# Performance work log

Hardware: AMD Instinct MI355X
Metric: run time of the kernel (lower is better)

Reference implementation:

```python
import jax, jax.numpy as jnp
import numpy as np

QLEN, BSZ, D_MODEL = 1024, 4, 1024
N_HEAD, D_HEAD = 16, 64
NEG = -1e30


def _layer_norm(x, g, b, eps=1e-5):
    mu = jnp.mean(x, axis=-1, keepdims=True)
    var = jnp.mean((x - mu) ** 2, axis=-1, keepdims=True)
    return (x - mu) / jnp.sqrt(var + eps) * g + b


def _rel_shift(x):
    # x: [qlen, klen, bsz, n_head] -- Transformer-XL relative shift
    q, k, b, n = x.shape
    x = jnp.pad(x, ((0, 0), (1, 0), (0, 0), (0, 0)))  # zero-pad along klen front
    x = x.reshape(k + 1, q, b, n)[1:]
    return x.reshape(q, k, b, n)


def setup_inputs() -> dict:
    key = jax.random.key(0)
    ks = jax.random.split(key, 8)
    s = 0.02
    w = jax.random.normal(ks[0], (QLEN, BSZ, D_MODEL), jnp.float32)
    r = jax.random.normal(ks[1], (QLEN, D_MODEL), jnp.float32)
    r_w_bias = jax.random.normal(ks[2], (N_HEAD, D_HEAD), jnp.float32) * s
    r_r_bias = jax.random.normal(ks[3], (N_HEAD, D_HEAD), jnp.float32) * s
    attn_mask = jnp.tril(jnp.ones((QLEN, QLEN), dtype=bool))  # causal: True = attend
    W_qkv = jax.random.normal(ks[4], (D_MODEL, 3 * N_HEAD * D_HEAD), jnp.float32) * s
    W_r = jax.random.normal(ks[5], (D_MODEL, N_HEAD * D_HEAD), jnp.float32) * s
    W_o = jax.random.normal(ks[6], (N_HEAD * D_HEAD, D_MODEL), jnp.float32) * s
    gamma = jnp.ones((D_MODEL,), jnp.float32)
    beta = jnp.zeros((D_MODEL,), jnp.float32)
    return {"w": w, "r": r, "r_w_bias": r_w_bias, "r_r_bias": r_r_bias,
            "attn_mask": attn_mask, "W_qkv": W_qkv, "W_r": W_r, "W_o": W_o,
            "gamma": gamma, "beta": beta}


def reference(w, r, r_w_bias, r_r_bias, attn_mask, W_qkv, W_r, W_o, gamma, beta):
    qlen, bsz, _ = w.shape
    scale = 1.0 / (D_HEAD ** 0.5)
    heads = w @ W_qkv                                    # [q, b, 3*n*d]
    q_h, k_h, v_h = jnp.split(heads, 3, axis=-1)
    q_h = q_h.reshape(qlen, bsz, N_HEAD, D_HEAD)
    k_h = k_h.reshape(qlen, bsz, N_HEAD, D_HEAD)
    v_h = v_h.reshape(qlen, bsz, N_HEAD, D_HEAD)
    r_k = (r @ W_r).reshape(-1, N_HEAD, D_HEAD)          # [rlen, n, d]
    AC = jnp.einsum('ibnd,jbnd->ijbn', q_h + r_w_bias, k_h)
    BD = jnp.einsum('ibnd,jnd->ijbn', q_h + r_r_bias, r_k)
    BD = _rel_shift(BD)
    score = (AC + BD) * scale                            # [q, k, b, n]
    score = jnp.where(attn_mask[:, :, None, None], score, NEG)
    prob = jax.nn.softmax(score, axis=1)
    vec = jnp.einsum('ijbn,jbnd->ibnd', prob, v_h).reshape(qlen, bsz, N_HEAD * D_HEAD)
    attn_out = vec @ W_o
    return _layer_norm(w + attn_out, gamma, beta)
```

## Files before the change

kernel.cpp:

```cpp
#include <hip/hip_runtime.h>
#include <math.h>

constexpr int QLEN_C  = 1024;
constexpr int BSZ_C   = 4;
constexpr int DMODEL  = 1024;
constexpr float SCALE = 0.125f;
constexpr float NEGF  = -1e30f;

typedef __attribute__((ext_vector_type(8))) short bh8;
typedef __attribute__((ext_vector_type(4))) float f32x4;

__device__ inline short f2bf(float f) {
    union { float f; unsigned u; } v; v.f = f;
    unsigned r = v.u + 0x7FFFu + ((v.u >> 16) & 1u);
    return (short)(r >> 16);
}
__device__ inline float bf2f(short s) {
    union { unsigned u; float f; } v;
    v.u = ((unsigned)(unsigned short)s) << 16;
    return v.f;
}
__device__ inline void gload16(const void* g, void* l) {
    __builtin_amdgcn_global_load_lds(
        (__attribute__((address_space(1))) void*)g,
        (__attribute__((address_space(3))) void*)l, 16, 0, 0);
}
__device__ inline void wave_lds_fence() {
    __builtin_amdgcn_sched_barrier(0);
    __builtin_amdgcn_s_waitcnt(0xC07F);
    __builtin_amdgcn_sched_barrier(0);
}
__device__ inline void block_sync() {
    __builtin_amdgcn_sched_barrier(0);
    __builtin_amdgcn_s_barrier();
    __builtin_amdgcn_sched_barrier(0);
}
__device__ inline void wait_vm8() {
    __builtin_amdgcn_sched_barrier(0);
    asm volatile("s_waitcnt vmcnt(8)" ::: "memory");
    __builtin_amdgcn_sched_barrier(0);
}
__device__ inline void wait_vm6() {
    __builtin_amdgcn_sched_barrier(0);
    asm volatile("s_waitcnt vmcnt(6)" ::: "memory");
    __builtin_amdgcn_sched_barrier(0);
}
__device__ inline void wait_vm0() {
    __builtin_amdgcn_sched_barrier(0);
    asm volatile("s_waitcnt vmcnt(0)" ::: "memory");
    __builtin_amdgcn_sched_barrier(0);
}

__global__ __launch_bounds__(512, 2)
void gemm12_8ph(const short* __restrict__ wb, const short* __restrict__ WqkvT,
                short* __restrict__ headsb,
                const short* __restrict__ rb, const short* __restrict__ WrT,
                short* __restrict__ rkb)
{
    constexpr int NT = 16;
    __shared__ alignas(16) short Ald[2][2][128][64];
    __shared__ alignas(16) short Bld[2][2][128][64];

    const int bid0 = blockIdx.x;
    const int bid = (bid0 & 7) * 26 + (bid0 >> 3);

    const short* A; const short* BT; short* Cc; int Nn; int bx, by;
    if (bid < 192) {
        A = wb; BT = WqkvT; Cc = headsb; Nn = 3072;
        bx = bid % 12; by = bid / 12;
    } else {
        int q = bid - 192;
        A = rb; BT = WrT; Cc = rkb; Nn = 1024;
        bx = q & 3; by = q >> 2;
    }
    const int row0 = by * 256, col0 = bx * 256;

    const int tid = threadIdx.x;
    const int wid = tid >> 6, lane = tid & 63;
    const int quad = lane >> 4, c = lane & 15;
    const int wr = wid >> 2, wcn = wid & 3;
    const int hb = wcn >> 1;

    auto stage_half = [&](short* dst, const short* src, int srcRow0, int kcol) {
        const int r0 = tid >> 3, b0 = tid & 7;
        gload16(src + (size_t)(srcRow0 + r0) * 1024 + kcol + ((b0 ^ (r0 & 7)) * 8),
                (char*)dst + tid * 16);
        const int t2 = tid + 512;
        const int r1 = t2 >> 3, b1 = t2 & 7;
        gload16(src + (size_t)(srcRow0 + r1) * 1024 + kcol + ((b1 ^ (r1 & 7)) * 8),
                (char*)dst + t2 * 16);
    };

    f32x4 acc[8][4];
    #pragma unroll
    for (int mf = 0; mf < 8; ++mf)
        #pragma unroll
        for (int nf = 0; nf < 4; ++nf) acc[mf][nf] = (f32x4)0.0f;

    stage_half(&Ald[0][0][0][0], A, row0,        0);
    stage_half(&Ald[0][1][0][0], A, row0 + 128,  0);
    stage_half(&Bld[0][0][0][0], BT, col0,       0);
    stage_half(&Bld[0][1][0][0], BT, col0 + 128, 0);
    stage_half(&Ald[1][0][0][0], A, row0,        64);
    stage_half(&Ald[1][1][0][0], A, row0 + 128,  64);
    stage_half(&Bld[1][0][0][0], BT, col0,       64);
    stage_half(&Bld[1][1][0][0], BT, col0 + 128, 64);
    wait_vm8();
    block_sync();

    for (int t = 0; t < NT; ++t) {
        const int d = t & 1;

        bh8 aF[8][2], bF[4][2];
        #pragma unroll
        for (int mf = 0; mf < 8; ++mf)
            #pragma unroll
            for (int ks = 0; ks < 2; ++ks)
                aF[mf][ks] = *(const bh8*)&Ald[d][wr][mf * 16 + c]
                                 [((ks * 4 + quad) ^ (c & 7)) * 8];
        #pragma unroll
        for (int nf = 0; nf < 4; ++nf)
            #pragma unroll
            for (int ks = 0; ks < 2; ++ks)
                bF[nf][ks] = *(const bh8*)&Bld[d][hb][(wcn & 1) * 64 + nf * 16 + c]
                                 [((ks * 4 + quad) ^ (c & 7)) * 8];

        wave_lds_fence();
        block_sync();

        const int ts = t + 2;

        __builtin_amdgcn_s_setprio(1);
        #pragma unroll
        for (int mf = 0; mf < 4; ++mf)
            #pragma unroll
            for (int nf = 0; nf < 2; ++nf) {
                acc[mf][nf] = __builtin_amdgcn_mfma_f32_16x16x32_bf16(aF[mf][0], bF[nf][0], acc[mf][nf], 0, 0, 0);
                acc[mf][nf] = __builtin_amdgcn_mfma_f32_16x16x32_bf16(aF[mf][1], bF[nf][1], acc[mf][nf], 0, 0, 0);
            }
        __builtin_amdgcn_s_setprio(0);

        if (ts < NT) {
            stage_half(&Ald[d][0][0][0], A, row0,       ts * 64);
            stage_half(&Ald[d][1][0][0], A, row0 + 128, ts * 64);
        }

        __builtin_amdgcn_s_setprio(1);
        #pragma unroll
        for (int mf = 0; mf < 4; ++mf)
            #pragma unroll
            for (int nf = 2; nf < 4; ++nf) {
                acc[mf][nf] = __builtin_amdgcn_mfma_f32_16x16x32_bf16(aF[mf][0], bF[nf][0], acc[mf][nf], 0, 0, 0);
                acc[mf][nf] = __builtin_amdgcn_mfma_f32_16x16x32_bf16(aF[mf][1], bF[nf][1], acc[mf][nf], 0, 0, 0);
            }
        __builtin_amdgcn_s_setprio(0);

        if (ts < NT) {
            stage_half(&Bld[d][0][0][0], BT, col0,       ts * 64);
            stage_half(&Bld[d][1][0][0], BT, col0 + 128, ts * 64);
        }

        __builtin_amdgcn_s_setprio(1);
        #pragma unroll
        for (int mf = 4; mf < 8; ++mf)
            #pragma unroll
            for (int nf = 0; nf < 2; ++nf) {
                acc[mf][nf] = __builtin_amdgcn_mfma_f32_16x16x32_bf16(aF[mf][0], bF[nf][0], acc[mf][nf], 0, 0, 0);
                acc[mf][nf] = __builtin_amdgcn_mfma_f32_16x16x32_bf16(aF[mf][1], bF[nf][1], acc[mf][nf], 0, 0, 0);
            }
        #pragma unroll
        for (int mf = 4; mf < 8; ++mf)
            #pragma unroll
            for (int nf = 2; nf < 4; ++nf) {
                acc[mf][nf] = __builtin_amdgcn_mfma_f32_16x16x32_bf16(aF[mf][0], bF[nf][0], acc[mf][nf], 0, 0, 0);
                acc[mf][nf] = __builtin_amdgcn_mfma_f32_16x16x32_bf16(aF[mf][1], bF[nf][1], acc[mf][nf], 0, 0, 0);
            }
        __builtin_amdgcn_s_setprio(0);

        if (t + 2 < NT)      wait_vm8();
        else if (t + 1 < NT) wait_vm0();
        if (t + 1 < NT)      block_sync();
    }

    wave_lds_fence();
    block_sync();
    short* cst = &Ald[0][0][0][0];
    const int crow = tid >> 2, cseg = tid & 3;
    #pragma unroll
    for (int pass = 0; pass < 2; ++pass) {
        if (wr == pass) {
            #pragma unroll
            for (int mf = 0; mf < 8; ++mf)
                #pragma unroll
                for (int nf = 0; nf < 4; ++nf)
                    #pragma unroll
                    for (int rr = 0; rr < 4; ++rr)
                        cst[(mf * 16 + quad * 4 + rr) * 256 + wcn * 64 + nf * 16 + c] =
                            f2bf(acc[mf][nf][rr]);
        }
        wave_lds_fence();
        block_sync();
        {
            short* gp = Cc + (size_t)(row0 + pass * 128 + crow) * Nn + col0 + cseg * 64;
            const short* lp = &cst[crow * 256 + cseg * 64];
            #pragma unroll
            for (int u = 0; u < 8; ++u)
                *(bh8*)(gp + u * 8) = *(const bh8*)(lp + u * 8);
        }
        if (pass == 0) { wave_lds_fence(); block_sync(); }
    }
}

__global__ __launch_bounds__(512, 2)
void gemm_wo_8ph(const short* __restrict__ A, const short* __restrict__ BT,
                 float* __restrict__ C0, float* __restrict__ C1)
{
    constexpr int NT = 8;
    constexpr int N  = 1024;
    __shared__ alignas(16) short Ald[2][2][128][64];
    __shared__ alignas(16) short Bld[2][128][64];

    const int bid0 = blockIdx.x;
    const int bid = (bid0 & 7) * 32 + (bid0 >> 3);
    const int half = bid & 1, tile = bid >> 1;
    const int by = tile >> 3, bx = tile & 7;
    const int row0 = by * 256, col0 = bx * 128;
    const int k_lo = half * 512;
    float* C = half ? C1 : C0;

    const int tid = threadIdx.x;
    const int wid = tid >> 6, lane = tid & 63;
    const int quad = lane >> 4, c = lane & 15;
    const int wr = wid >> 2, wcn = wid & 3;

    auto stage_half = [&](short* dst, const short* src, int srcRow0, int kcol) {
        const int r0 = tid >> 3, b0 = tid & 7;
        gload16(src + (size_t)(srcRow0 + r0) * 1024 + kcol + ((b0 ^ (r0 & 7)) * 8),
                (char*)dst + tid * 16);
        const int t2 = tid + 512;
        const int r1 = t2 >> 3, b1 = t2 & 7;
        gload16(src + (size_t)(srcRow0 + r1) * 1024 + kcol + ((b1 ^ (r1 & 7)) * 8),
                (char*)dst + t2 * 16);
    };

    f32x4 acc[8][2];
    #pragma unroll
    for (int mf = 0; mf < 8; ++mf)
        #pragma unroll
        for (int nf = 0; nf < 2; ++nf) acc[mf][nf] = (f32x4)0.0f;

    stage_half(&Ald[0][0][0][0], A, row0,        k_lo);
    stage_half(&Ald[0][1][0][0], A, row0 + 128,  k_lo);
    stage_half(&Bld[0][0][0],    BT, col0,       k_lo);
    stage_half(&Ald[1][0][0][0], A, row0,        k_lo + 64);
    stage_half(&Ald[1][1][0][0], A, row0 + 128,  k_lo + 64);
    stage_half(&Bld[1][0][0],    BT, col0,       k_lo + 64);
    wait_vm6();
    block_sync();

    for (int t = 0; t < NT; ++t) {
        const int d = t & 1;

        bh8 aF[8][2], bF[2][2];
        #pragma unroll
        for (int mf = 0; mf < 8; ++mf)
            #pragma unroll
            for (int ks = 0; ks < 2; ++ks)
                aF[mf][ks] = *(const bh8*)&Ald[d][wr][mf * 16 + c]
                                 [((ks * 4 + quad) ^ (c & 7)) * 8];
        #pragma unroll
        for (int nf = 0; nf < 2; ++nf)
            #pragma unroll
            for (int ks = 0; ks < 2; ++ks)
                bF[nf][ks] = *(const bh8*)&Bld[d][wcn * 32 + nf * 16 + c]
                                 [((ks * 4 + quad) ^ (c & 7)) * 8];

        wave_lds_fence();
        block_sync();

        const int ts = t + 2;
        const int kc = k_lo + ts * 64;

        __builtin_amdgcn_s_setprio(1);
        #pragma unroll
        for (int mf = 0; mf < 4; ++mf)
            #pragma unroll
            for (int nf = 0; nf < 2; ++nf) {
                acc[mf][nf] = __builtin_amdgcn_mfma_f32_16x16x32_bf16(aF[mf][0], bF[nf][0], acc[mf][nf], 0, 0, 0);
                acc[mf][nf] = __builtin_amdgcn_mfma_f32_16x16x32_bf16(aF[mf][1], bF[nf][1], acc[mf][nf], 0, 0, 0);
            }
        __builtin_amdgcn_s_setprio(0);

        if (ts < NT) {
            stage_half(&Ald[d][0][0][0], A, row0,       kc);
            stage_half(&Ald[d][1][0][0], A, row0 + 128, kc);
        }

        __builtin_amdgcn_s_setprio(1);
        #pragma unroll
        for (int mf = 4; mf < 6; ++mf)
            #pragma unroll
            for (int nf = 0; nf < 2; ++nf) {
                acc[mf][nf] = __builtin_amdgcn_mfma_f32_16x16x32_bf16(aF[mf][0], bF[nf][0], acc[mf][nf], 0, 0, 0);
                acc[mf][nf] = __builtin_amdgcn_mfma_f32_16x16x32_bf16(aF[mf][1], bF[nf][1], acc[mf][nf], 0, 0, 0);
            }
        __builtin_amdgcn_s_setprio(0);

        if (ts < NT) stage_half(&Bld[d][0][0], BT, col0, kc);

        __builtin_amdgcn_s_setprio(1);
        #pragma unroll
        for (int mf = 6; mf < 8; ++mf)
            #pragma unroll
            for (int nf = 0; nf < 2; ++nf) {
                acc[mf][nf] = __builtin_amdgcn_mfma_f32_16x16x32_bf16(aF[mf][0], bF[nf][0], acc[mf][nf], 0, 0, 0);
                acc[mf][nf] = __builtin_amdgcn_mfma_f32_16x16x32_bf16(aF[mf][1], bF[nf][1], acc[mf][nf], 0, 0, 0);
            }
        __builtin_amdgcn_s_setprio(0);

        if (t + 2 < NT)      wait_vm6();
        else if (t + 1 < NT) wait_vm0();
        if (t + 1 < NT)      block_sync();
    }

    #pragma unroll
    for (int mf = 0; mf < 8; ++mf)
        #pragma unroll
        for (int nf = 0; nf < 2; ++nf)
            #pragma unroll
            for (int rr = 0; rr < 4; ++rr) {
                int orow = row0 + wr * 128 + mf * 16 + quad * 4 + rr;
                int ocol = col0 + wcn * 32 + nf * 16 + c;
                C[(size_t)orow * N + ocol] = acc[mf][nf][rr];
            }
}

__device__ inline void transp_tile(const float* __restrict__ B, short* __restrict__ BT,
                                   int K, int N, int n0, int k0, int t,
                                   float (*tile)[68])
{
    const int row = t >> 2, c4 = t & 3;
    const float* src = B + (size_t)(k0 + row) * N + n0 + c4 * 16;
    #pragma unroll
    for (int u = 0; u < 4; ++u) {
        float4 v = *(const float4*)(src + u * 4);
        tile[row][c4 * 16 + u * 4 + 0] = v.x;
        tile[row][c4 * 16 + u * 4 + 1] = v.y;
        tile[row][c4 * 16 + u * 4 + 2] = v.z;
        tile[row][c4 * 16 + u * 4 + 3] = v.w;
    }
    __syncthreads();
    const int nl = t >> 2, kc = t & 3;
    short tmp[16];
    #pragma unroll
    for (int e = 0; e < 16; ++e) tmp[e] = f2bf(tile[kc * 16 + e][nl]);
    short* dst = BT + (size_t)(n0 + nl) * K + k0 + kc * 16;
    *(bh8*)dst = *(bh8*)&tmp[0];
    *(bh8*)(dst + 8) = *(bh8*)&tmp[8];
}

__global__ __launch_bounds__(256)
void prep_all(const float* __restrict__ w, const float* __restrict__ r,
              const float* __restrict__ Wqkv, const float* __restrict__ Wr,
              const float* __restrict__ Wo,
              short* __restrict__ wb, short* __restrict__ rb,
              short* __restrict__ WqkvT, short* __restrict__ WrT,
              short* __restrict__ WoT, short* __restrict__ rkb)
{
    __shared__ float tile[64][68];
    const int bid = blockIdx.x;
    const int t = threadIdx.x;

    if (bid < 2048) {
        int idx = (bid * 256 + t) * 8;
        bh8 o;
        #pragma unroll
        for (int e = 0; e < 8; ++e) o[e] = f2bf(w[idx + e]);
        *(bh8*)(wb + idx) = o;
    } else if (bid < 2560) {
        int idx = ((bid - 2048) * 256 + t) * 8;
        bh8 o;
        #pragma unroll
        for (int e = 0; e < 8; ++e) o[e] = f2bf(r[idx + e]);
        *(bh8*)(rb + idx) = o;
    } else if (bid < 3328) {
        int tt = bid - 2560;
        transp_tile(Wqkv, WqkvT, 1024, 3072, (tt % 48) * 64, (tt / 48) * 64, t, tile);
    } else if (bid < 3584) {
        int tt = bid - 3328;
        transp_tile(Wr, WrT, 1024, 1024, (tt % 16) * 64, (tt / 16) * 64, t, tile);
    } else if (bid < 3840) {
        int tt = bid - 3584;
        transp_tile(Wo, WoT, 1024, 1024, (tt % 16) * 64, (tt / 16) * 64, t, tile);
    } else {
        int idx = 1024 * 1024 + ((bid - 3840) * 256 + t) * 8;
        bh8 z;
        #pragma unroll
        for (int e = 0; e < 8; ++e) z[e] = 0;
        *(bh8*)(rkb + idx) = z;
    }
}

__global__ __launch_bounds__(256)
void prep_kv2(const short* __restrict__ headsb, const short* __restrict__ rkb,
              short* __restrict__ kfrag, short* __restrict__ vfrag,
              short* __restrict__ rfrag)
{
    __shared__ short vtile[64][72];
    const int blk = blockIdx.x;
    const int t = threadIdx.x;

    if (blk < 1024) {
        const int bn = blk >> 4, ju = blk & 15;
        const int b = bn & 3, nn = bn >> 2;
        const int j0 = ju * 64;
        const int row = t >> 2, d0 = (t & 3) * 16;

        const short* kp = headsb + ((size_t)(j0 + row) * 4 + b) * 3072 + 1024 + nn * 64 + d0;
        const short* vp = kp + 1024;
        bh8 k0 = *(const bh8*)kp, k1 = *(const bh8*)(kp + 8);
        bh8 v0 = *(const bh8*)vp, v1 = *(const bh8*)(vp + 8);

        {
            const int jtile = (j0 + row) >> 4, cc = row & 15;
            short* kb_bn = kfrag + (size_t)bn * 65536 + (size_t)jtile * 1024 + cc * 8;
            const int d1 = d0 + 8;
            *(bh8*)(kb_bn + (d0 >> 5) * 512 + ((d0 >> 3) & 3) * 128) = k0;
            *(bh8*)(kb_bn + (d1 >> 5) * 512 + ((d1 >> 3) & 3) * 128) = k1;
        }
        #pragma unroll
        for (int e = 0; e < 8; ++e) {
            vtile[row][d0 + e] = v0[e];
            vtile[row][d0 + 8 + e] = v1[e];
        }
        __syncthreads();
        const int d = t >> 2, jl0 = (t & 3) * 16;
        short tmp[16];
        #pragma unroll
        for (int e = 0; e < 16; ++e) tmp[e] = vtile[jl0 + e][d];
        short* vb = vfrag + (size_t)bn * 65536 + (size_t)ju * 4096
                  + (d >> 4) * 1024 + (d & 15) * 8;
        const int jl1 = jl0 + 8;
        *(bh8*)(vb + (jl0 >> 5) * 512 + ((jl0 >> 3) & 3) * 128) = *(bh8*)&tmp[0];
        *(bh8*)(vb + (jl1 >> 5) * 512 + ((jl1 >> 3) & 3) * 128) = *(bh8*)&tmp[8];
    } else {
        const int rblk = blk - 1024;
        const int row = rblk * 4 + (t >> 6);
        const int col0 = (t & 63) * 16;
        const short* src = rkb + (size_t)row * 1024 + col0;
        bh8 r0 = *(const bh8*)src, r1 = *(const bh8*)(src + 8);
        const int rt = row >> 4, cc = row & 15;
        const int nn = col0 >> 6, dd = col0 & 63, dd1 = dd + 8;
        short* dst = rfrag + (size_t)rt * 16384 + nn * 1024 + cc * 8;
        *(bh8*)(dst + (dd  >> 5) * 512 + ((dd  >> 3) & 3) * 128) = r0;
        *(bh8*)(dst + (dd1 >> 5) * 512 + ((dd1 >> 3) & 3) * 128) = r1;
    }
}

__global__ __launch_bounds__(256)
void attn_mfma(const short* __restrict__ headsb, const short* __restrict__ rfrag,
               const short* __restrict__ kfrag, const short* __restrict__ vfrag,
               const float* __restrict__ rwb, const float* __restrict__ rrb,
               short* __restrict__ vecb)
{
    __shared__ alignas(16) short sP[4][2][16 * 80];

    const int tid = threadIdx.x;
    const int wave = tid >> 6, lane = tid & 63;
    const int quad = lane >> 4, c = lane & 15;

    const int bi = blockIdx.x;
    const int itile = 15 - (bi >> 6);
    const int bn = bi & 63;
    const int n = bn >> 2, b = bn & 3;
    const int nU = itile + 1;
    const int rb = itile * 64 + wave * 16;

    const int dq = n * 64 + quad * 8;
    const short* kbp = kfrag + (size_t)bn * 65536;
    const short* vtp = vfrag + (size_t)bn * 65536;
    const int lin = quad * 128 + c * 8;

    bh8 ones;
    #pragma unroll
    for (int e = 0; e < 8; ++e) ones[e] = (short)0x3F80;

    bh8 aAC[2], aBD[2];
    #pragma unroll
    for (int ks = 0; ks < 2; ++ks) {
        const short* qp = headsb + ((size_t)(rb + c) * 4 + b) * 3072 + dq + 32 * ks;
        bh8 q8 = *(const bh8*)qp;
        #pragma unroll
        for (int e = 0; e < 8; ++e) {
            float qv = bf2f(q8[e]);
            aAC[ks][e] = f2bf(qv + rwb[dq + 32 * ks + e]);
            aBD[ks][e] = f2bf(qv + rrb[dq + 32 * ks + e]);
        }
    }

    bh8 rkv[10], kbv[8];
    auto pf = [&](int j0) {
        const int rt0 = (1008 - rb + j0) >> 4;
        #pragma unroll
        for (int tt = 0; tt < 5; ++tt) {
            const short* rp = rfrag + (size_t)(rt0 + tt) * 16384 + n * 1024 + lin;
            rkv[2 * tt]     = *(const bh8*)rp;
            rkv[2 * tt + 1] = *(const bh8*)(rp + 512);
        }
        const int jt0 = j0 >> 4;
        #pragma unroll
        for (int jt = 0; jt < 4; ++jt) {
            const short* kp = kbp + (size_t)(jt0 + jt) * 1024 + lin;
            kbv[2 * jt]     = *(const bh8*)kp;
            kbv[2 * jt + 1] = *(const bh8*)(kp + 512);
        }
    };

    f32x4 oacc[4], lacc;
    #pragma unroll
    for (int dt = 0; dt < 4; ++dt) oacc[dt] = (f32x4)0.0f;
    lacc = (f32x4)0.0f;

    pf(0);
    int j0 = 0;

    for (int u = 0; u < nU; ++u) {
        short* PL = &sP[wave][u & 1][0];

        bh8 vvv[8];
        {
            const short* vup = vtp + (size_t)(j0 >> 6) * 4096;
            #pragma unroll
            for (int dt = 0; dt < 4; ++dt) {
                const short* vp = vup + dt * 1024 + lin;
                vvv[2 * dt]     = *(const bh8*)vp;
                vvv[2 * dt + 1] = *(const bh8*)(vp + 512);
            }
        }

        f32x4 bt[5];
        #pragma unroll
        for (int tt = 0; tt < 5; ++tt) {
            bt[tt] = (f32x4)0.0f;
            bt[tt] = __builtin_amdgcn_mfma_f32_16x16x32_bf16(aBD[0], rkv[2 * tt], bt[tt], 0, 0, 0);
            bt[tt] = __builtin_amdgcn_mfma_f32_16x16x32_bf16(aBD[1], rkv[2 * tt + 1], bt[tt], 0, 0, 0);
        }
        f32x4 ac[4];
        #pragma unroll
        for (int jt = 0; jt < 4; ++jt) {
            ac[jt] = (f32x4)0.0f;
            ac[jt] = __builtin_amdgcn_mfma_f32_16x16x32_bf16(aAC[0], kbv[2 * jt], ac[jt], 0, 0, 0);
            ac[jt] = __builtin_amdgcn_mfma_f32_16x16x32_bf16(aAC[1], kbv[2 * jt + 1], ac[jt], 0, 0, 0);
        }

        if (u + 1 < nU) pf(j0 + 64);

        #pragma unroll
        for (int r = 0; r < 4; ++r) {
            const int row = quad * 4 + r;
            const int o = 15 - row;
            const int src = (lane & 48) | ((c + o) & 15);
            const int gi = rb + row;
            #pragma unroll
            for (int jt = 0; jt < 4; ++jt) {
                float sval = (c < o) ? bt[jt + 1][r] : bt[jt][r];
                float bd = __shfl(sval, src, 64);
                int gj = j0 + c + 16 * jt;
                float v = SCALE * (ac[jt][r] + bd);
                PL[row * 80 + c + 16 * jt] = (gj > gi) ? (short)0 : f2bf(__expf(v));
            }
        }

        wave_lds_fence();

        bh8 aP[2];
        #pragma unroll
        for (int ks = 0; ks < 2; ++ks)
            aP[ks] = *(const bh8*)(PL + c * 80 + 32 * ks + quad * 8);
        #pragma unroll
        for (int dt = 0; dt < 4; ++dt) {
            oacc[dt] = __builtin_amdgcn_mfma_f32_16x16x32_bf16(aP[0], vvv[2 * dt], oacc[dt], 0, 0, 0);
            oacc[dt] = __builtin_amdgcn_mfma_f32_16x16x32_bf16(aP[1], vvv[2 * dt + 1], oacc[dt], 0, 0, 0);
        }
        lacc = __builtin_amdgcn_mfma_f32_16x16x32_bf16(aP[0], ones, lacc, 0, 0, 0);
        lacc = __builtin_amdgcn_mfma_f32_16x16x32_bf16(aP[1], ones, lacc, 0, 0, 0);

        j0 += 64;
    }

    #pragma unroll
    for (int r = 0; r < 4; ++r) {
        float rinv = 1.f / lacc[r];
        int gi = rb + quad * 4 + r;
        short* op = vecb + ((size_t)gi * 4 + b) * 1024 + n * 64;
        #pragma unroll
        for (int dt = 0; dt < 4; ++dt)
            op[c + 16 * dt] = f2bf(oacc[dt][r] * rinv);
    }
}

__global__ __launch_bounds__(256)
void ln_kernel(const float* __restrict__ w, const float* __restrict__ a0,
               const float* __restrict__ a1,
               const float* __restrict__ gamma, const float* __restrict__ beta,
               float* __restrict__ out)
{
    const int row = blockIdx.x;
    const int tid = threadIdx.x;
    const float4* xw4 = (const float4*)(w  + (size_t)row * DMODEL);
    const float4* p04 = (const float4*)(a0 + (size_t)row * DMODEL);
    const float4* p14 = (const float4*)(a1 + (size_t)row * DMODEL);

    float4 a = xw4[tid], b0 = p04[tid], b1 = p14[tid];
    float x[4] = {a.x + b0.x + b1.x, a.y + b0.y + b1.y,
                  a.z + b0.z + b1.z, a.w + b0.w + b1.w};
    float s = x[0] + x[1] + x[2] + x[3];

    __shared__ float red[6];
    #pragma unroll
    for (int m = 1; m < 64; m <<= 1) s += __shfl_xor(s, m, 64);
    int wv = tid >> 6, lnid = tid & 63;
    if (lnid == 0) red[wv] = s;
    __syncthreads();
    if (tid == 0) red[4] = red[0] + red[1] + red[2] + red[3];
    __syncthreads();
    float mu = red[4] * (1.f / DMODEL);

    float vs = 0.f;
    #pragma unroll
    for (int e = 0; e < 4; ++e) { float d = x[e] - mu; vs += d * d; }
    #pragma unroll
    for (int m = 1; m < 64; m <<= 1) vs += __shfl_xor(vs, m, 64);
    if (lnid == 0) red[wv] = vs;
    __syncthreads();
    if (tid == 0) red[5] = red[0] + red[1] + red[2] + red[3];
    __syncthreads();
    float var = red[5] * (1.f / DMODEL);
    float inv = rsqrtf(var + 1e-5f);

    float4 g = ((const float4*)gamma)[tid];
    float4 be = ((const float4*)beta)[tid];
    float4 o;
    o.x = (x[0] - mu) * inv * g.x + be.x;
    o.y = (x[1] - mu) * inv * g.y + be.y;
    o.z = (x[2] - mu) * inv * g.z + be.z;
    o.w = (x[3] - mu) * inv * g.w + be.w;
    ((float4*)(out + (size_t)row * DMODEL))[tid] = o;
}

extern "C" void kernel_launch(void* const* d_in, const int* in_sizes, int n_in,
                              void* d_out, int out_size, void* d_ws, size_t ws_size,
                              hipStream_t stream)
{
    const float* w     = (const float*)d_in[0];
    const float* r     = (const float*)d_in[1];
    const float* rwb   = (const float*)d_in[2];
    const float* rrb   = (const float*)d_in[3];
    const float* Wqkv  = (const float*)d_in[5];
    const float* Wr    = (const float*)d_in[6];
    const float* Wo    = (const float*)d_in[7];
    const float* gamma = (const float*)d_in[8];
    const float* beta  = (const float*)d_in[9];
    float* out = (float*)d_out;

    short* headsb = (short*)d_ws;
    short* wb     = headsb + 12582912;
    short* WqkvT  = wb + 4194304;
    short* rb     = WqkvT + 3145728;
    short* WrT    = rb + 1048576;
    short* WoT    = WrT + 1048576;
    short* rkb    = WoT + 1048576;
    short* kfrag  = rkb + 1114112;
    short* vfrag  = kfrag + 4194304;
    short* vecb   = vfrag + 4194304;

    short* rfrag  = rb;

    float* attno0 = (float*)headsb;
    float* attno1 = (float*)wb;

    prep_all<<<3872, 256, 0, stream>>>(w, r, Wqkv, Wr, Wo, wb, rb, WqkvT, WrT, WoT, rkb);
    gemm12_8ph<<<dim3(208), 512, 0, stream>>>(wb, WqkvT, headsb, rb, WrT, rkb);
    prep_kv2<<<dim3(1296), 256, 0, stream>>>(headsb, rkb, kfrag, vfrag, rfrag);
    attn_mfma<<<dim3(1024), 256, 0, stream>>>(headsb, rfrag, kfrag, vfrag, rwb, rrb, vecb);
    gemm_wo_8ph<<<dim3(256), 512, 0, stream>>>(vecb, WoT, attno0, attno1);
    ln_kernel<<<4096, 256, 0, stream>>>(w, attno0, attno1, gamma, beta, out);
}
```

Before: 127.6 us.

## Split long causal attention rows into two KV halves and combine partials

Query tiles 8-15 now have their key range split into two tasks, giving 24 tasks per head/batch instead of 16. The split tasks write unnormalized partial outputs and row sums to scratch, and a new combine kernel adds them and normalizes. The aim is to balance the triangular workload across the grid and shorten the tail of long-row blocks. It also moves the causal mask check onto the diagonal tile only, and rearranges the rfrag fragments in place instead of copying them. The cost is an extra launch plus fp32 partial traffic; the in-place shuffle relies on each block only touching its own tile.

```diff
diff --git a/kernel.cpp b/kernel.cpp
--- a/kernel.cpp
+++ b/kernel.cpp
@@ -5,7 +5,6 @@
 constexpr int BSZ_C   = 4;
 constexpr int DMODEL  = 1024;
 constexpr float SCALE = 0.125f;
-constexpr float NEGF  = -1e30f;
 
 typedef __attribute__((ext_vector_type(8))) short bh8;
 typedef __attribute__((ext_vector_type(4))) float f32x4;
@@ -402,9 +401,8 @@
 }
 
 __global__ __launch_bounds__(256)
-void prep_kv2(const short* __restrict__ headsb, const short* __restrict__ rkb,
-              short* __restrict__ kfrag, short* __restrict__ vfrag,
-              short* __restrict__ rfrag)
+void prep_kv2(const short* __restrict__ headsb, short* __restrict__ rfrag,
+              short* __restrict__ kfrag, short* __restrict__ vfrag)
 {
     __shared__ short vtile[64][72];
     const int blk = blockIdx.x;
@@ -444,24 +442,33 @@
         *(bh8*)(vb + (jl0 >> 5) * 512 + ((jl0 >> 3) & 3) * 128) = *(bh8*)&tmp[0];
         *(bh8*)(vb + (jl1 >> 5) * 512 + ((jl1 >> 3) & 3) * 128) = *(bh8*)&tmp[8];
     } else {
-        const int rblk = blk - 1024;
-        const int row = rblk * 4 + (t >> 6);
-        const int col0 = (t & 63) * 16;
-        const short* src = rkb + (size_t)row * 1024 + col0;
-        bh8 r0 = *(const bh8*)src, r1 = *(const bh8*)(src + 8);
-        const int rt = row >> 4, cc = row & 15;
-        const int nn = col0 >> 6, dd = col0 & 63, dd1 = dd + 8;
-        short* dst = rfrag + (size_t)rt * 16384 + nn * 1024 + cc * 8;
-        *(bh8*)(dst + (dd  >> 5) * 512 + ((dd  >> 3) & 3) * 128) = r0;
-        *(bh8*)(dst + (dd1 >> 5) * 512 + ((dd1 >> 3) & 3) * 128) = r1;
-    }
-}
+        const int rt = blk - 1024;
+        short* base = rfrag + (size_t)rt * 16384;
+        const int cc = t >> 4, nn = t & 15;
+        const short* src = base + cc * 1024 + nn * 64;
+        bh8 v[8];
+        #pragma unroll
+        for (int i = 0; i < 8; ++i) v[i] = *(const bh8*)(src + i * 8);
+        __syncthreads();
+        short* dst = base + nn * 1024 + cc * 8;
+        #pragma unroll
+        for (int ks = 0; ks < 2; ++ks)
+            #pragma unroll
+            for (int qb = 0; qb < 4; ++qb)
+                *(bh8*)(dst + ks * 512 + qb * 128) = v[ks * 4 + qb];
+    }
+}
+
+__device__ __constant__ int T_IT[24] = {7,14,15,15, 6,12,13,13,14, 5,10,11,11,12, 4,8,9,9,10, 3,8, 2, 1, 0};
+__device__ __constant__ int T_U0[24] = {0, 0, 0, 8, 0, 0, 0, 7, 8, 0, 0, 0, 6, 7, 0,0,0,5,6, 0,5, 0, 0, 0};
+__device__ __constant__ int T_U1[24] = {8, 8, 8,16, 7, 7, 7,14,15, 6, 6, 6,12,13, 5,5,5,10,11, 4,9, 3, 2, 1};
 
 __global__ __launch_bounds__(256)
 void attn_mfma(const short* __restrict__ headsb, const short* __restrict__ rfrag,
                const short* __restrict__ kfrag, const short* __restrict__ vfrag,
                const float* __restrict__ rwb, const float* __restrict__ rrb,
-               short* __restrict__ vecb)
+               short* __restrict__ vecb,
+               float* __restrict__ Opart, float* __restrict__ lpart)
 {
     __shared__ alignas(16) short sP[4][2][16 * 80];
 
@@ -470,10 +477,13 @@
     const int quad = lane >> 4, c = lane & 15;
 
     const int bi = blockIdx.x;
-    const int itile = 15 - (bi >> 6);
+    const int task = bi >> 6;
     const int bn = bi & 63;
+    const int itile = T_IT[task];
+    const int u0 = T_U0[task], u1 = T_U1[task];
     const int n = bn >> 2, b = bn & 3;
-    const int nU = itile + 1;
+    const int nU = u1 - u0;
+    const bool diag = (u1 == itile + 1);
     const int rb = itile * 64 + wave * 16;
 
     const int dq = n * 64 + quad * 8;
@@ -521,8 +531,8 @@
     for (int dt = 0; dt < 4; ++dt) oacc[dt] = (f32x4)0.0f;
     lacc = (f32x4)0.0f;
 
-    pf(0);
-    int j0 = 0;
+    int j0 = u0 * 64;
+    pf(j0);
 
     for (int u = 0; u < nU; ++u) {
         short* PL = &sP[wave][u & 1][0];
@@ -555,19 +565,24 @@
 
         if (u + 1 < nU) pf(j0 + 64);
 
+        const bool maskedU = diag && (u == nU - 1);
         #pragma unroll
         for (int r = 0; r < 4; ++r) {
             const int row = quad * 4 + r;
             const int o = 15 - row;
             const int src = (lane & 48) | ((c + o) & 15);
-            const int gi = rb + row;
             #pragma unroll
             for (int jt = 0; jt < 4; ++jt) {
                 float sval = (c < o) ? bt[jt + 1][r] : bt[jt][r];
                 float bd = __shfl(sval, src, 64);
-                int gj = j0 + c + 16 * jt;
                 float v = SCALE * (ac[jt][r] + bd);
-                PL[row * 80 + c + 16 * jt] = (gj > gi) ? (short)0 : f2bf(__expf(v));
+                short pv = f2bf(__expf(v));
+                if (maskedU) {
+                    int gj = j0 + c + 16 * jt;
+                    int gi = rb + row;
+                    if (gj > gi) pv = 0;
+                }
+                PL[row * 80 + c + 16 * jt] = pv;
             }
         }
 
@@ -588,15 +603,64 @@
         j0 += 64;
     }
 
-    #pragma unroll
-    for (int r = 0; r < 4; ++r) {
-        float rinv = 1.f / lacc[r];
-        int gi = rb + quad * 4 + r;
-        short* op = vecb + ((size_t)gi * 4 + b) * 1024 + n * 64;
-        #pragma unroll
-        for (int dt = 0; dt < 4; ++dt)
-            op[c + 16 * dt] = f2bf(oacc[dt][r] * rinv);
-    }
+    if (itile < 8) {
+        #pragma unroll
+        for (int r = 0; r < 4; ++r) {
+            float rinv = 1.f / lacc[r];
+            int gi = rb + quad * 4 + r;
+            short* op = vecb + ((size_t)gi * 4 + b) * 1024 + n * 64;
+            #pragma unroll
+            for (int dt = 0; dt < 4; ++dt)
+                op[c + 16 * dt] = f2bf(oacc[dt][r] * rinv);
+        }
+    } else {
+        const int pid = itile - 8;
+        const int half = (u0 != 0);
+        const size_t base = (size_t)((bn * 8 + pid) * 2 + half);
+        float* Ob = Opart + base * 4096;
+        float* lb = lpart + base * 64;
+        #pragma unroll
+        for (int r = 0; r < 4; ++r) {
+            const int wrow = wave * 16 + quad * 4 + r;
+            #pragma unroll
+            for (int dt = 0; dt < 4; ++dt)
+                Ob[wrow * 64 + c + 16 * dt] = oacc[dt][r];
+            if (c == 0) lb[wrow] = lacc[r];
+        }
+    }
+}
+
+__global__ __launch_bounds__(256)
+void combine_att(const float* __restrict__ Op, const float* __restrict__ lp,
+                 short* __restrict__ vecb)
+{
+    const int bp = blockIdx.x;
+    const int bn = bp >> 3, pid = bp & 7;
+    const int n = bn >> 2, b = bn & 3;
+    const int t = threadIdx.x;
+    const int row = t >> 2, d0 = (t & 3) * 16;
+
+    const float* O0 = Op + ((size_t)(bp * 2 + 0)) * 4096 + row * 64 + d0;
+    const float* O1 = Op + ((size_t)(bp * 2 + 1)) * 4096 + row * 64 + d0;
+    const float l0 = lp[(size_t)(bp * 2 + 0) * 64 + row];
+    const float l1 = lp[(size_t)(bp * 2 + 1) * 64 + row];
+    const float rinv = 1.f / (l0 + l1);
+
+    const int gi = (pid + 8) * 64 + row;
+    short* op = vecb + ((size_t)gi * 4 + b) * 1024 + n * 64 + d0;
+
+    short tmp[16];
+    #pragma unroll
+    for (int q = 0; q < 4; ++q) {
+        float4 v0 = *(const float4*)(O0 + q * 4);
+        float4 v1 = *(const float4*)(O1 + q * 4);
+        tmp[q * 4 + 0] = f2bf((v0.x + v1.x) * rinv);
+        tmp[q * 4 + 1] = f2bf((v0.y + v1.y) * rinv);
+        tmp[q * 4 + 2] = f2bf((v0.z + v1.z) * rinv);
+        tmp[q * 4 + 3] = f2bf((v0.w + v1.w) * rinv);
+    }
+    *(bh8*)op = *(bh8*)&tmp[0];
+    *(bh8*)(op + 8) = *(bh8*)&tmp[8];
 }
 
 __global__ __launch_bounds__(256)
@@ -674,15 +738,20 @@
     short* vfrag  = kfrag + 4194304;
     short* vecb   = vfrag + 4194304;
 
-    short* rfrag  = rb;
+    short* rfrag  = rkb;
+
+    float* Opart  = (float*)wb;
+    float* lpart  = Opart + 4194304;
 
     float* attno0 = (float*)headsb;
     float* attno1 = (float*)wb;
 
     prep_all<<<3872, 256, 0, stream>>>(w, r, Wqkv, Wr, Wo, wb, rb, WqkvT, WrT, WoT, rkb);
     gemm12_8ph<<<dim3(208), 512, 0, stream>>>(wb, WqkvT, headsb, rb, WrT, rkb);
-    prep_kv2<<<dim3(1296), 256, 0, stream>>>(headsb, rkb, kfrag, vfrag, rfrag);
-    attn_mfma<<<dim3(1024), 256, 0, stream>>>(headsb, rfrag, kfrag, vfrag, rwb, rrb, vecb);
+    prep_kv2<<<dim3(1092), 256, 0, stream>>>(headsb, rfrag, kfrag, vfrag);
+    attn_mfma<<<dim3(1536), 256, 0, stream>>>(headsb, rfrag, kfrag, vfrag,
+                                              rwb, rrb, vecb, Opart, lpart);
+    combine_att<<<dim3(512), 256, 0, stream>>>(Opart, lpart, vecb);
     gemm_wo_8ph<<<dim3(256), 512, 0, stream>>>(vecb, WoT, attno0, attno1);
     ln_kernel<<<4096, 256, 0, stream>>>(w, attno0, attno1, gamma, beta, out);
 }
```

Measured after the change: 134.2 us. +5.1%, slower.
